# Optimization experiments

Measured on AMD Instinct MI355X. Metric: run time of the kernel, lower is better.

Reference implementation:

```python
import jax, jax.numpy as jnp
import numpy as np

# NOTE: in the original SelfAttention.forward, the selected/softmaxed/dropped
# attention `attn` is NEVER used: the output is `torch.matmul(attn_cont, value)`
# with the RAW pre-mask, pre-softmax, unscaled scores. The AutoSelectAttention /
# softmax / dropout branch is dead code w.r.t. the module output, so the faithful
# forward is out = proj_out( (Q K^T) V ) per head.

B, M, HID, K = 2, 2048, 1024, 16
D = HID // K


def setup_inputs() -> dict:
    key = jax.random.key(0)
    ks = jax.random.split(key, 6)
    s = 1.0 / np.sqrt(HID)
    return {
        "h": jax.random.normal(ks[0], (B, M, HID), jnp.float32),
        "Wq": jax.random.normal(ks[1], (HID, HID), jnp.float32) * s,
        "Wk": jax.random.normal(ks[2], (HID, HID), jnp.float32) * s,
        "Wv": jax.random.normal(ks[3], (HID, HID), jnp.float32) * s,
        "Wspan": jax.random.normal(ks[4], (2 * K, HID), jnp.float32) * s,
        "Wo": jax.random.normal(ks[5], (HID, HID), jnp.float32) * s,
    }


def _heads(x, d):
    # [B, M, K*d] -> [B, K, M, d]
    b, m, _ = x.shape
    return x.reshape(b, m, K, d).transpose(0, 2, 1, 3)


def reference(h, Wq, Wk, Wv, Wspan, Wo):
    # torch Linear: y = x @ W.T  (weights stored [out, in])
    q = _heads(h @ Wq.T, D)          # [B,K,M,D]
    k = _heads(h @ Wk.T, D)          # [B,K,M,D]
    v = _heads(h @ Wv.T, D)          # [B,K,M,D]
    span = _heads(h @ Wspan.T, 2)    # [B,K,M,2] -- dead code in original, kept for parity
    del span
    # raw scores (attn_cont in the original)
    scores = jnp.einsum("bkmd,bknd->bkmn", q, k)      # [B,K,M,M]
    # original: out = attn_cont @ value (select/softmax branch unused)
    out = jnp.einsum("bkmn,bknd->bkmd", scores, v)    # [B,K,M,D]
    out = out.transpose(0, 2, 1, 3).reshape(B, M, HID)
    return out @ Wo.T
```

## Files before the change

kernel.cpp:

```cpp
#include <hip/hip_runtime.h>
#include <hip/hip_bf16.h>
#include <stdint.h>

typedef __hip_bfloat16 bf16_t;
typedef __attribute__((ext_vector_type(8))) __bf16 bf16x8;
typedef __attribute__((ext_vector_type(4))) float floatx4;

#define BM 128
#define BN 128
#define BK 64

__device__ inline void async_load16(const void* g, void* l) {
  __builtin_amdgcn_global_load_lds(
      (const __attribute__((address_space(1))) unsigned int*)g,
      (__attribute__((address_space(3))) unsigned int*)l,
      16, 0, 0);
}

__device__ inline unsigned short bf16_bits(float f) {
  bf16_t b = __float2bfloat16(f);
  return *(const unsigned short*)&b;
}

__global__ void cvt_one(const float* __restrict__ src, bf16_t* __restrict__ dst) {
  const int i = (blockIdx.x * 256 + threadIdx.x) * 4;
  float4 f = *(const float4*)(src + i);
  union { unsigned short u[4]; uint2 v; } p;
  p.u[0] = bf16_bits(f.x); p.u[1] = bf16_bits(f.y);
  p.u[2] = bf16_bits(f.z); p.u[3] = bf16_bits(f.w);
  *(uint2*)(dst + i) = p.v;
}

__global__ void cvt_w4(const float* __restrict__ s0, const float* __restrict__ s1,
                       const float* __restrict__ s2, const float* __restrict__ s3,
                       bf16_t* __restrict__ d0, bf16_t* __restrict__ d1,
                       bf16_t* __restrict__ d2, bf16_t* __restrict__ d3) {
  const float* s; bf16_t* d;
  switch (blockIdx.y) {
    case 0: s = s0; d = d0; break;
    case 1: s = s1; d = d1; break;
    case 2: s = s2; d = d2; break;
    default: s = s3; d = d3; break;
  }
  const int i = (blockIdx.x * 256 + threadIdx.x) * 4;
  float4 f = *(const float4*)(s + i);
  union { unsigned short u[4]; uint2 v; } p;
  p.u[0] = bf16_bits(f.x); p.u[1] = bf16_bits(f.y);
  p.u[2] = bf16_bits(f.z); p.u[3] = bf16_bits(f.w);
  *(uint2*)(d + i) = p.v;
}

template <typename OutT, bool TKV>
__global__ __launch_bounds__(256, 2)
void gemm_nt(const bf16_t* __restrict__ A, int lda,
             const bf16_t* __restrict__ B0, const bf16_t* __restrict__ B1,
             const bf16_t* __restrict__ B2,
             OutT* __restrict__ C, int ldc, int Kdim,
             bf16_t* __restrict__ Kt, bf16_t* __restrict__ Vt)
{
  __shared__ alignas(16) __bf16 As[BM * BK];
  __shared__ alignas(16) __bf16 Bs[BN * BK];

  const int t = threadIdx.x;
  const int lane = t & 63;
  const int wave = t >> 6;
  const int wm = wave >> 1;
  const int wn = wave & 1;

  const int m0 = blockIdx.x * BM;
  const int nblk = blockIdx.y * BN;
  const int mat = nblk >> 10;
  const bf16_t* __restrict__ B = (mat == 0) ? B0 : ((mat == 1) ? B1 : B2);
  const int n0 = nblk & 1023;

  floatx4 acc[4][4];
#pragma unroll
  for (int i = 0; i < 4; ++i)
#pragma unroll
    for (int j = 0; j < 4; ++j)
      acc[i][j] = (floatx4){0.f, 0.f, 0.f, 0.f};

  const int srow = t >> 3;
  const int sgs = t & 7;

  for (int k0 = 0; k0 < Kdim; k0 += BK) {
#pragma unroll
    for (int r4 = 0; r4 < 4; ++r4) {
      const int row = r4 * 32 + srow;
      const int gsrc = sgs ^ (row & 7);
      async_load16(A + (size_t)(m0 + row) * lda + k0 + gsrc * 8,
                   &As[row * BK + sgs * 8]);
      async_load16(B + (size_t)(n0 + row) * Kdim + k0 + gsrc * 8,
                   &Bs[row * BK + sgs * 8]);
    }
    __syncthreads();
#pragma unroll
    for (int ks = 0; ks < 2; ++ks) {
      bf16x8 af[4], bfv[4];
#pragma unroll
      for (int i = 0; i < 4; ++i) {
        const int row = wm * 64 + i * 16 + (lane & 15);
        const int g = ks * 4 + (lane >> 4);
        af[i] = *(const bf16x8*)&As[row * BK + (g ^ (row & 7)) * 8];
      }
#pragma unroll
      for (int j = 0; j < 4; ++j) {
        const int row = wn * 64 + j * 16 + (lane & 15);
        const int g = ks * 4 + (lane >> 4);
        bfv[j] = *(const bf16x8*)&Bs[row * BK + (g ^ (row & 7)) * 8];
      }
#pragma unroll
      for (int i = 0; i < 4; ++i)
#pragma unroll
        for (int j = 0; j < 4; ++j)
          acc[i][j] = __builtin_amdgcn_mfma_f32_16x16x32_bf16(
              af[i], bfv[j], acc[i][j], 0, 0, 0);
    }
    __syncthreads();
  }

  const int ccol = lane & 15;
  const int crow = (lane >> 4) * 4;

  if constexpr (TKV) {
    if (mat != 0) {
      bf16_t* __restrict__ T = (mat == 1) ? Kt : Vt;
#pragma unroll
      for (int i = 0; i < 4; ++i) {
#pragma unroll
        for (int j = 0; j < 4; ++j) {
          const int lc = n0 + wn * 64 + j * 16 + ccol;
          const int hidx = lc >> 6, d = lc & 63;
          const int grow = m0 + wm * 64 + i * 16 + crow;
          const int bidx = grow >> 11, mloc = grow & 2047;
          union { unsigned short u[4]; uint2 v; } p;
#pragma unroll
          for (int r = 0; r < 4; ++r) p.u[r] = bf16_bits(acc[i][j][r]);
          *(uint2*)(T + (((size_t)bidx * 16 + hidx) * 64 + d) * 2048 + mloc) = p.v;
        }
      }
      return;
    }
  }

#pragma unroll
  for (int i = 0; i < 4; ++i) {
#pragma unroll
    for (int j = 0; j < 4; ++j) {
      const int gcol = n0 + wn * 64 + j * 16 + ccol;
      const int growb = m0 + wm * 64 + i * 16 + crow;
#pragma unroll
      for (int r = 0; r < 4; ++r) {
        float v = acc[i][j][r];
        if constexpr (__is_same(OutT, bf16_t))
          C[(size_t)(growb + r) * ldc + gcol] = __float2bfloat16(v);
        else
          C[(size_t)(growb + r) * ldc + gcol] = v;
      }
    }
  }
}

__global__ __launch_bounds__(256, 2)
void ktv_gemm(const bf16_t* __restrict__ Kt, const bf16_t* __restrict__ Vt,
              float* __restrict__ St)
{
  __shared__ alignas(16) __bf16 As[64 * 64];
  __shared__ alignas(16) __bf16 Bs[64 * 64];

  const int t = threadIdx.x;
  const int lane = t & 63;
  const int wave = t >> 6;
  const int bh = blockIdx.x;
  const int kc = blockIdx.y;

  const bf16_t* A = Vt + (size_t)bh * 64 * 2048;
  const bf16_t* B = Kt + (size_t)bh * 64 * 2048;

  floatx4 acc[4];
#pragma unroll
  for (int j = 0; j < 4; ++j) acc[j] = (floatx4){0.f, 0.f, 0.f, 0.f};

  const int srow = t >> 3;
  const int sgs = t & 7;

  for (int k0 = kc * 256; k0 < kc * 256 + 256; k0 += 64) {
#pragma unroll
    for (int r2 = 0; r2 < 2; ++r2) {
      const int row = r2 * 32 + srow;
      const int gsrc = sgs ^ (row & 7);
      async_load16(A + (size_t)row * 2048 + k0 + gsrc * 8, &As[row * 64 + sgs * 8]);
      async_load16(B + (size_t)row * 2048 + k0 + gsrc * 8, &Bs[row * 64 + sgs * 8]);
    }
    __syncthreads();
#pragma unroll
    for (int ks = 0; ks < 2; ++ks) {
      bf16x8 af, bfv[4];
      {
        const int row = wave * 16 + (lane & 15);
        const int g = ks * 4 + (lane >> 4);
        af = *(const bf16x8*)&As[row * 64 + (g ^ (row & 7)) * 8];
      }
#pragma unroll
      for (int j = 0; j < 4; ++j) {
        const int row = j * 16 + (lane & 15);
        const int g = ks * 4 + (lane >> 4);
        bfv[j] = *(const bf16x8*)&Bs[row * 64 + (g ^ (row & 7)) * 8];
      }
#pragma unroll
      for (int j = 0; j < 4; ++j)
        acc[j] = __builtin_amdgcn_mfma_f32_16x16x32_bf16(af, bfv[j], acc[j], 0, 0, 0);
    }
    __syncthreads();
  }

  const int ccol = lane & 15;
  const int crow = (lane >> 4) * 4;
  float* Sp = St + (size_t)bh * 4096;
#pragma unroll
  for (int j = 0; j < 4; ++j)
#pragma unroll
    for (int r = 0; r < 4; ++r)
      unsafeAtomicAdd(&Sp[(wave * 16 + crow + r) * 64 + j * 16 + ccol], acc[j][r]);
}

__global__ __launch_bounds__(256, 2)
void qs_mfma(const bf16_t* __restrict__ Qbuf, const float* __restrict__ St,
             bf16_t* __restrict__ O)
{
  __shared__ alignas(16) __bf16 Qs[128 * 64];
  __shared__ alignas(16) __bf16 Sb[64 * 64];

  const int t = threadIdx.x;
  const int lane = t & 63;
  const int wave = t >> 6;
  const int bh = blockIdx.x;
  const int b = bh >> 4, hh = bh & 15;
  const int mt = blockIdx.y;

  const bf16_t* qbase = Qbuf + (size_t)(b * 2048 + mt * 128) * 1024 + hh * 64;
  const int srow = t >> 3;
  const int sgs = t & 7;
#pragma unroll
  for (int r4 = 0; r4 < 4; ++r4) {
    const int row = r4 * 32 + srow;
    const int gsrc = sgs ^ (row & 7);
    async_load16(qbase + (size_t)row * 1024 + gsrc * 8, &Qs[row * 64 + sgs * 8]);
  }
  {
    const int r = t >> 2;
    const int g0 = (t & 3) * 2;
    const float* sp = St + (size_t)bh * 4096 + r * 64;
#pragma unroll
    for (int gg = 0; gg < 2; ++gg) {
      const int g = g0 + gg;
      const int gs = g ^ (r & 7);
      const float4 f0 = *(const float4*)(sp + gs * 8);
      const float4 f1 = *(const float4*)(sp + gs * 8 + 4);
      union { unsigned short u[8]; uint4 v; } pk;
      pk.u[0] = bf16_bits(f0.x); pk.u[1] = bf16_bits(f0.y);
      pk.u[2] = bf16_bits(f0.z); pk.u[3] = bf16_bits(f0.w);
      pk.u[4] = bf16_bits(f1.x); pk.u[5] = bf16_bits(f1.y);
      pk.u[6] = bf16_bits(f1.z); pk.u[7] = bf16_bits(f1.w);
      *(uint4*)&Sb[r * 64 + g * 8] = pk.v;
    }
  }
  __syncthreads();

  floatx4 acc[2][4];
#pragma unroll
  for (int i = 0; i < 2; ++i)
#pragma unroll
    for (int j = 0; j < 4; ++j)
      acc[i][j] = (floatx4){0.f, 0.f, 0.f, 0.f};

#pragma unroll
  for (int ks = 0; ks < 2; ++ks) {
    bf16x8 af[2], bfv[4];
#pragma unroll
    for (int i = 0; i < 2; ++i) {
      const int row = wave * 32 + i * 16 + (lane & 15);
      const int g = ks * 4 + (lane >> 4);
      af[i] = *(const bf16x8*)&Qs[row * 64 + (g ^ (row & 7)) * 8];
    }
#pragma unroll
    for (int j = 0; j < 4; ++j) {
      const int row = j * 16 + (lane & 15);
      const int g = ks * 4 + (lane >> 4);
      bfv[j] = *(const bf16x8*)&Sb[row * 64 + (g ^ (row & 7)) * 8];
    }
#pragma unroll
    for (int i = 0; i < 2; ++i)
#pragma unroll
      for (int j = 0; j < 4; ++j)
        acc[i][j] = __builtin_amdgcn_mfma_f32_16x16x32_bf16(
            af[i], bfv[j], acc[i][j], 0, 0, 0);
  }

  const int ccol = lane & 15;
  const int crow = (lane >> 4) * 4;
#pragma unroll
  for (int i = 0; i < 2; ++i) {
#pragma unroll
    for (int j = 0; j < 4; ++j) {
      const int col = hh * 64 + j * 16 + ccol;
      const int mrow = mt * 128 + wave * 32 + i * 16 + crow;
#pragma unroll
      for (int r = 0; r < 4; ++r)
        O[(size_t)(b * 2048 + mrow + r) * 1024 + col] = __float2bfloat16(acc[i][j][r]);
    }
  }
}

extern "C" void kernel_launch(void* const* d_in, const int* in_sizes, int n_in,
                              void* d_out, int out_size, void* d_ws, size_t ws_size,
                              hipStream_t stream)
{
  const float* h  = (const float*)d_in[0];
  const float* Wq = (const float*)d_in[1];
  const float* Wk = (const float*)d_in[2];
  const float* Wv = (const float*)d_in[3];
  const float* Wo = (const float*)d_in[5];
  float* out = (float*)d_out;

  char* ws = (char*)d_ws;
  bf16_t* hb   = (bf16_t*)(ws);
  bf16_t* Obuf = (bf16_t*)(ws);
  bf16_t* Wqb  = (bf16_t*)(ws + (8u << 20));
  bf16_t* Wkb  = (bf16_t*)(ws + (10u << 20));
  bf16_t* Wvb  = (bf16_t*)(ws + (12u << 20));
  bf16_t* Wob  = (bf16_t*)(ws + (14u << 20));
  bf16_t* Qbuf = (bf16_t*)(ws + (16u << 20));
  bf16_t* Kt   = (bf16_t*)(ws + (24u << 20));
  bf16_t* Vt   = (bf16_t*)(ws + (32u << 20));
  float*  St   = (float*) (ws + (40u << 20));

  hipMemsetAsync(St, 0, 32 * 64 * 64 * sizeof(float), stream);

  cvt_one<<<dim3(4096), 256, 0, stream>>>(h, hb);
  cvt_w4<<<dim3(1024, 4), 256, 0, stream>>>(Wq, Wk, Wv, Wo, Wqb, Wkb, Wvb, Wob);

  gemm_nt<bf16_t, true><<<dim3(32, 24), 256, 0, stream>>>(
      hb, 1024, Wqb, Wkb, Wvb, Qbuf, 1024, 1024, Kt, Vt);
  ktv_gemm<<<dim3(32, 8), 256, 0, stream>>>(Kt, Vt, St);
  qs_mfma<<<dim3(32, 16), 256, 0, stream>>>(Qbuf, St, Obuf);
  gemm_nt<float, false><<<dim3(32, 8), 256, 0, stream>>>(
      Obuf, 1024, Wob, Wob, Wob, out, 1024, 1024, nullptr, nullptr);
}
```

Baseline: 148.4 us.

## Fold per-head K^T V state into output projection weights before final GEMM

Reassociates the computation so each head's 64x64 K^T V matrix is multiplied into Wo, producing a per-batch effective weight. The final GEMM then reads Q and that effective weight directly, which removes the Q·S intermediate pass and its buffer round-trip. The final GEMM is split-K by two with atomic adds into a zeroed output. The conversion kernels and the S memset are merged into one launch. The cost is an extra memset of the output, atomic accumulation traffic, and a different bf16 rounding point for the fused weights.

```diff
diff --git a/kernel.cpp b/kernel.cpp
--- a/kernel.cpp
+++ b/kernel.cpp
@@ -22,27 +22,29 @@
   return *(const unsigned short*)&b;
 }
 
-__global__ void cvt_one(const float* __restrict__ src, bf16_t* __restrict__ dst) {
-  const int i = (blockIdx.x * 256 + threadIdx.x) * 4;
-  float4 f = *(const float4*)(src + i);
-  union { unsigned short u[4]; uint2 v; } p;
-  p.u[0] = bf16_bits(f.x); p.u[1] = bf16_bits(f.y);
-  p.u[2] = bf16_bits(f.z); p.u[3] = bf16_bits(f.w);
-  *(uint2*)(dst + i) = p.v;
-}
-
-__global__ void cvt_w4(const float* __restrict__ s0, const float* __restrict__ s1,
-                       const float* __restrict__ s2, const float* __restrict__ s3,
-                       bf16_t* __restrict__ d0, bf16_t* __restrict__ d1,
-                       bf16_t* __restrict__ d2, bf16_t* __restrict__ d3) {
-  const float* s; bf16_t* d;
-  switch (blockIdx.y) {
-    case 0: s = s0; d = d0; break;
-    case 1: s = s1; d = d1; break;
-    case 2: s = s2; d = d2; break;
-    default: s = s3; d = d3; break;
-  }
-  const int i = (blockIdx.x * 256 + threadIdx.x) * 4;
+__global__ void cvt_all(const float* __restrict__ h, const float* __restrict__ Wq,
+                        const float* __restrict__ Wk, const float* __restrict__ Wv,
+                        const float* __restrict__ Wo,
+                        bf16_t* __restrict__ hb, bf16_t* __restrict__ Wqb,
+                        bf16_t* __restrict__ Wkb, bf16_t* __restrict__ Wvb,
+                        bf16_t* __restrict__ Wob, float* __restrict__ S)
+{
+  const int bid = blockIdx.x;
+  if (bid >= 8192) {
+    float4* s4 = (float4*)S;
+    const int base = (bid - 8192) * 256 + threadIdx.x;
+#pragma unroll
+    for (int i = 0; i < 64; ++i)
+      s4[base + i * 512] = (float4){0.f, 0.f, 0.f, 0.f};
+    return;
+  }
+  const float* s; bf16_t* d; int base;
+  if (bid < 4096)      { s = h;  d = hb;  base = bid; }
+  else if (bid < 5120) { s = Wq; d = Wqb; base = bid - 4096; }
+  else if (bid < 6144) { s = Wk; d = Wkb; base = bid - 5120; }
+  else if (bid < 7168) { s = Wv; d = Wvb; base = bid - 6144; }
+  else                 { s = Wo; d = Wob; base = bid - 7168; }
+  const int i = (base * 256 + threadIdx.x) * 4;
   float4 f = *(const float4*)(s + i);
   union { unsigned short u[4]; uint2 v; } p;
   p.u[0] = bf16_bits(f.x); p.u[1] = bf16_bits(f.y);
@@ -50,13 +52,12 @@
   *(uint2*)(d + i) = p.v;
 }
 
-template <typename OutT, bool TKV>
 __global__ __launch_bounds__(256, 2)
-void gemm_nt(const bf16_t* __restrict__ A, int lda,
-             const bf16_t* __restrict__ B0, const bf16_t* __restrict__ B1,
-             const bf16_t* __restrict__ B2,
-             OutT* __restrict__ C, int ldc, int Kdim,
-             bf16_t* __restrict__ Kt, bf16_t* __restrict__ Vt)
+void gemm_qkv(const bf16_t* __restrict__ A, int lda,
+              const bf16_t* __restrict__ B0, const bf16_t* __restrict__ B1,
+              const bf16_t* __restrict__ B2,
+              bf16_t* __restrict__ Qbuf,
+              bf16_t* __restrict__ Kt, bf16_t* __restrict__ Vt)
 {
   __shared__ alignas(16) __bf16 As[BM * BK];
   __shared__ alignas(16) __bf16 Bs[BN * BK];
@@ -83,14 +84,14 @@
   const int srow = t >> 3;
   const int sgs = t & 7;
 
-  for (int k0 = 0; k0 < Kdim; k0 += BK) {
+  for (int k0 = 0; k0 < 1024; k0 += BK) {
 #pragma unroll
     for (int r4 = 0; r4 < 4; ++r4) {
       const int row = r4 * 32 + srow;
       const int gsrc = sgs ^ (row & 7);
       async_load16(A + (size_t)(m0 + row) * lda + k0 + gsrc * 8,
                    &As[row * BK + sgs * 8]);
-      async_load16(B + (size_t)(n0 + row) * Kdim + k0 + gsrc * 8,
+      async_load16(B + (size_t)(n0 + row) * 1024 + k0 + gsrc * 8,
                    &Bs[row * BK + sgs * 8]);
     }
     __syncthreads();
@@ -122,25 +123,23 @@
   const int ccol = lane & 15;
   const int crow = (lane >> 4) * 4;
 
-  if constexpr (TKV) {
-    if (mat != 0) {
-      bf16_t* __restrict__ T = (mat == 1) ? Kt : Vt;
-#pragma unroll
-      for (int i = 0; i < 4; ++i) {
-#pragma unroll
-        for (int j = 0; j < 4; ++j) {
-          const int lc = n0 + wn * 64 + j * 16 + ccol;
-          const int hidx = lc >> 6, d = lc & 63;
-          const int grow = m0 + wm * 64 + i * 16 + crow;
-          const int bidx = grow >> 11, mloc = grow & 2047;
-          union { unsigned short u[4]; uint2 v; } p;
-#pragma unroll
-          for (int r = 0; r < 4; ++r) p.u[r] = bf16_bits(acc[i][j][r]);
-          *(uint2*)(T + (((size_t)bidx * 16 + hidx) * 64 + d) * 2048 + mloc) = p.v;
-        }
-      }
-      return;
-    }
+  if (mat != 0) {
+    bf16_t* __restrict__ T = (mat == 1) ? Kt : Vt;
+#pragma unroll
+    for (int i = 0; i < 4; ++i) {
+#pragma unroll
+      for (int j = 0; j < 4; ++j) {
+        const int lc = n0 + wn * 64 + j * 16 + ccol;
+        const int hidx = lc >> 6, d = lc & 63;
+        const int grow = m0 + wm * 64 + i * 16 + crow;
+        const int bidx = grow >> 11, mloc = grow & 2047;
+        union { unsigned short u[4]; uint2 v; } p;
+#pragma unroll
+        for (int r = 0; r < 4; ++r) p.u[r] = bf16_bits(acc[i][j][r]);
+        *(uint2*)(T + (((size_t)bidx * 16 + hidx) * 64 + d) * 2048 + mloc) = p.v;
+      }
+    }
+    return;
   }
 
 #pragma unroll
@@ -150,20 +149,15 @@
       const int gcol = n0 + wn * 64 + j * 16 + ccol;
       const int growb = m0 + wm * 64 + i * 16 + crow;
 #pragma unroll
-      for (int r = 0; r < 4; ++r) {
-        float v = acc[i][j][r];
-        if constexpr (__is_same(OutT, bf16_t))
-          C[(size_t)(growb + r) * ldc + gcol] = __float2bfloat16(v);
-        else
-          C[(size_t)(growb + r) * ldc + gcol] = v;
-      }
+      for (int r = 0; r < 4; ++r)
+        Qbuf[(size_t)(growb + r) * 1024 + gcol] = __float2bfloat16(acc[i][j][r]);
     }
   }
 }
 
 __global__ __launch_bounds__(256, 2)
 void ktv_gemm(const bf16_t* __restrict__ Kt, const bf16_t* __restrict__ Vt,
-              float* __restrict__ St)
+              float* __restrict__ S)
 {
   __shared__ alignas(16) __bf16 As[64 * 64];
   __shared__ alignas(16) __bf16 Bs[64 * 64];
@@ -174,8 +168,8 @@
   const int bh = blockIdx.x;
   const int kc = blockIdx.y;
 
-  const bf16_t* A = Vt + (size_t)bh * 64 * 2048;
-  const bf16_t* B = Kt + (size_t)bh * 64 * 2048;
+  const bf16_t* A = Kt + (size_t)bh * 64 * 2048;
+  const bf16_t* B = Vt + (size_t)bh * 64 * 2048;
 
   floatx4 acc[4];
 #pragma unroll
@@ -216,7 +210,7 @@
 
   const int ccol = lane & 15;
   const int crow = (lane >> 4) * 4;
-  float* Sp = St + (size_t)bh * 4096;
+  float* Sp = S + (size_t)bh * 4096;
 #pragma unroll
   for (int j = 0; j < 4; ++j)
 #pragma unroll
@@ -225,10 +219,10 @@
 }
 
 __global__ __launch_bounds__(256, 2)
-void qs_mfma(const bf16_t* __restrict__ Qbuf, const float* __restrict__ St,
-             bf16_t* __restrict__ O)
-{
-  __shared__ alignas(16) __bf16 Qs[128 * 64];
+void weff_mfma(const bf16_t* __restrict__ Wob, const float* __restrict__ S,
+               bf16_t* __restrict__ WeffT)
+{
+  __shared__ alignas(16) __bf16 Aw[128 * 64];
   __shared__ alignas(16) __bf16 Sb[64 * 64];
 
   const int t = threadIdx.x;
@@ -236,21 +230,21 @@
   const int wave = t >> 6;
   const int bh = blockIdx.x;
   const int b = bh >> 4, hh = bh & 15;
-  const int mt = blockIdx.y;
-
-  const bf16_t* qbase = Qbuf + (size_t)(b * 2048 + mt * 128) * 1024 + hh * 64;
+  const int nt = blockIdx.y;
+
+  const bf16_t* wbase = Wob + (size_t)(nt * 128) * 1024 + hh * 64;
   const int srow = t >> 3;
   const int sgs = t & 7;
 #pragma unroll
   for (int r4 = 0; r4 < 4; ++r4) {
     const int row = r4 * 32 + srow;
     const int gsrc = sgs ^ (row & 7);
-    async_load16(qbase + (size_t)row * 1024 + gsrc * 8, &Qs[row * 64 + sgs * 8]);
+    async_load16(wbase + (size_t)row * 1024 + gsrc * 8, &Aw[row * 64 + sgs * 8]);
   }
   {
     const int r = t >> 2;
     const int g0 = (t & 3) * 2;
-    const float* sp = St + (size_t)bh * 4096 + r * 64;
+    const float* sp = S + (size_t)bh * 4096 + r * 64;
 #pragma unroll
     for (int gg = 0; gg < 2; ++gg) {
       const int g = g0 + gg;
@@ -281,7 +275,7 @@
     for (int i = 0; i < 2; ++i) {
       const int row = wave * 32 + i * 16 + (lane & 15);
       const int g = ks * 4 + (lane >> 4);
-      af[i] = *(const bf16x8*)&Qs[row * 64 + (g ^ (row & 7)) * 8];
+      af[i] = *(const bf16x8*)&Aw[row * 64 + (g ^ (row & 7)) * 8];
     }
 #pragma unroll
     for (int j = 0; j < 4; ++j) {
@@ -299,15 +293,95 @@
 
   const int ccol = lane & 15;
   const int crow = (lane >> 4) * 4;
+  bf16_t* Wt = WeffT + (size_t)b * 1024 * 1024;
 #pragma unroll
   for (int i = 0; i < 2; ++i) {
 #pragma unroll
     for (int j = 0; j < 4; ++j) {
-      const int col = hh * 64 + j * 16 + ccol;
-      const int mrow = mt * 128 + wave * 32 + i * 16 + crow;
+      const int hd = hh * 64 + j * 16 + ccol;
+      const int n = nt * 128 + wave * 32 + i * 16 + crow;
 #pragma unroll
       for (int r = 0; r < 4; ++r)
-        O[(size_t)(b * 2048 + mrow + r) * 1024 + col] = __float2bfloat16(acc[i][j][r]);
+        Wt[(size_t)(n + r) * 1024 + hd] = __float2bfloat16(acc[i][j][r]);
+    }
+  }
+}
+
+__global__ __launch_bounds__(256, 2)
+void gemm_final(const bf16_t* __restrict__ Q, const bf16_t* __restrict__ WeffT,
+                float* __restrict__ C)
+{
+  __shared__ alignas(16) __bf16 As[BM * BK];
+  __shared__ alignas(16) __bf16 Bs[BN * BK];
+
+  const int t = threadIdx.x;
+  const int lane = t & 63;
+  const int wave = t >> 6;
+  const int wm = wave >> 1;
+  const int wn = wave & 1;
+
+  const int m0 = blockIdx.x * BM;
+  const int n0 = blockIdx.y * BN;
+  const int kbase = blockIdx.z * 512;
+  const bf16_t* __restrict__ B = WeffT + (size_t)(m0 >> 11) * 1024 * 1024;
+
+  floatx4 acc[4][4];
+#pragma unroll
+  for (int i = 0; i < 4; ++i)
+#pragma unroll
+    for (int j = 0; j < 4; ++j)
+      acc[i][j] = (floatx4){0.f, 0.f, 0.f, 0.f};
+
+  const int srow = t >> 3;
+  const int sgs = t & 7;
+
+  for (int k0 = kbase; k0 < kbase + 512; k0 += BK) {
+#pragma unroll
+    for (int r4 = 0; r4 < 4; ++r4) {
+      const int row = r4 * 32 + srow;
+      const int gsrc = sgs ^ (row & 7);
+      async_load16(Q + (size_t)(m0 + row) * 1024 + k0 + gsrc * 8,
+                   &As[row * BK + sgs * 8]);
+      async_load16(B + (size_t)(n0 + row) * 1024 + k0 + gsrc * 8,
+                   &Bs[row * BK + sgs * 8]);
+    }
+    __syncthreads();
+#pragma unroll
+    for (int ks = 0; ks < 2; ++ks) {
+      bf16x8 af[4], bfv[4];
+#pragma unroll
+      for (int i = 0; i < 4; ++i) {
+        const int row = wm * 64 + i * 16 + (lane & 15);
+        const int g = ks * 4 + (lane >> 4);
+        af[i] = *(const bf16x8*)&As[row * BK + (g ^ (row & 7)) * 8];
+      }
+#pragma unroll
+      for (int j = 0; j < 4; ++j) {
+        const int row = wn * 64 + j * 16 + (lane & 15);
+        const int g = ks * 4 + (lane >> 4);
+        bfv[j] = *(const bf16x8*)&Bs[row * BK + (g ^ (row & 7)) * 8];
+      }
+#pragma unroll
+      for (int i = 0; i < 4; ++i)
+#pragma unroll
+        for (int j = 0; j < 4; ++j)
+          acc[i][j] = __builtin_amdgcn_mfma_f32_16x16x32_bf16(
+              af[i], bfv[j], acc[i][j], 0, 0, 0);
+    }
+    __syncthreads();
+  }
+
+  const int ccol = lane & 15;
+  const int crow = (lane >> 4) * 4;
+#pragma unroll
+  for (int i = 0; i < 4; ++i) {
+#pragma unroll
+    for (int j = 0; j < 4; ++j) {
+      const int gcol = n0 + wn * 64 + j * 16 + ccol;
+      const int grow = m0 + wm * 64 + i * 16 + crow;
+#pragma unroll
+      for (int r = 0; r < 4; ++r)
+        unsafeAtomicAdd(&C[(size_t)(grow + r) * 1024 + gcol], acc[i][j][r]);
     }
   }
 }
@@ -324,26 +398,22 @@
   float* out = (float*)d_out;
 
   char* ws = (char*)d_ws;
-  bf16_t* hb   = (bf16_t*)(ws);
-  bf16_t* Obuf = (bf16_t*)(ws);
-  bf16_t* Wqb  = (bf16_t*)(ws + (8u << 20));
-  bf16_t* Wkb  = (bf16_t*)(ws + (10u << 20));
-  bf16_t* Wvb  = (bf16_t*)(ws + (12u << 20));
-  bf16_t* Wob  = (bf16_t*)(ws + (14u << 20));
-  bf16_t* Qbuf = (bf16_t*)(ws + (16u << 20));
-  bf16_t* Kt   = (bf16_t*)(ws + (24u << 20));
-  bf16_t* Vt   = (bf16_t*)(ws + (32u << 20));
-  float*  St   = (float*) (ws + (40u << 20));
-
-  hipMemsetAsync(St, 0, 32 * 64 * 64 * sizeof(float), stream);
-
-  cvt_one<<<dim3(4096), 256, 0, stream>>>(h, hb);
-  cvt_w4<<<dim3(1024, 4), 256, 0, stream>>>(Wq, Wk, Wv, Wo, Wqb, Wkb, Wvb, Wob);
-
-  gemm_nt<bf16_t, true><<<dim3(32, 24), 256, 0, stream>>>(
-      hb, 1024, Wqb, Wkb, Wvb, Qbuf, 1024, 1024, Kt, Vt);
-  ktv_gemm<<<dim3(32, 8), 256, 0, stream>>>(Kt, Vt, St);
-  qs_mfma<<<dim3(32, 16), 256, 0, stream>>>(Qbuf, St, Obuf);
-  gemm_nt<float, false><<<dim3(32, 8), 256, 0, stream>>>(
-      Obuf, 1024, Wob, Wob, Wob, out, 1024, 1024, nullptr, nullptr);
-}
+  bf16_t* hb    = (bf16_t*)(ws);
+  bf16_t* WeffT = (bf16_t*)(ws);
+  bf16_t* Wqb   = (bf16_t*)(ws + (8u << 20));
+  bf16_t* Wkb   = (bf16_t*)(ws + (10u << 20));
+  bf16_t* Wvb   = (bf16_t*)(ws + (12u << 20));
+  bf16_t* Wob   = (bf16_t*)(ws + (14u << 20));
+  bf16_t* Qbuf  = (bf16_t*)(ws + (16u << 20));
+  bf16_t* Kt    = (bf16_t*)(ws + (24u << 20));
+  bf16_t* Vt    = (bf16_t*)(ws + (32u << 20));
+  float*  S     = (float*) (ws + (40u << 20));
+
+  cvt_all<<<dim3(8194), 256, 0, stream>>>(h, Wq, Wk, Wv, Wo, hb, Wqb, Wkb, Wvb, Wob, S);
+
+  gemm_qkv<<<dim3(32, 24), 256, 0, stream>>>(hb, 1024, Wqb, Wkb, Wvb, Qbuf, Kt, Vt);
+  ktv_gemm<<<dim3(32, 8), 256, 0, stream>>>(Kt, Vt, S);
+  weff_mfma<<<dim3(32, 8), 256, 0, stream>>>(Wob, S, WeffT);
+  hipMemsetAsync(out, 0, (size_t)4096 * 1024 * sizeof(float), stream);
+  gemm_final<<<dim3(32, 8, 2), 256, 0, stream>>>(Qbuf, WeffT, out);
+}
```

Result: slower. 167.4 us (+12.8%).
